# Kernel optimization log

Measured on AMD Instinct MI355X. Metric: run time of the kernel, lower is better.

The kernel has to match this reference:

```python
import jax, jax.numpy as jnp
import numpy as np
from jax import lax

SEQ_LEN = 1024
BATCH = 256
INPUT_SIZE = 64
STATE_SIZE = 960
STREAM_SIZE = INPUT_SIZE + STATE_SIZE  # 1024
OUTPUT_SIZE = 64
IDENTITY_PROPORTION = 0.97


def _xavier_uniform(key, shape):
    fan_in, fan_out = shape[1], shape[0]
    limit = np.sqrt(6.0 / (fan_in + fan_out)).astype(np.float32)
    return jax.random.uniform(key, shape, jnp.float32, -limit, limit)


def setup_inputs() -> dict:
    key = jax.random.key(0)
    k_x, k_w1, k_w2 = jax.random.split(key, 3)
    return {
        "input": jax.random.normal(k_x, (SEQ_LEN, BATCH, INPUT_SIZE), jnp.float32),
        "W1": _xavier_uniform(k_w1, (STREAM_SIZE, STREAM_SIZE)),
        "b1": jnp.zeros((STREAM_SIZE,), jnp.float32),
        "W2": _xavier_uniform(k_w2, (STREAM_SIZE, STREAM_SIZE)),
        "b2": jnp.zeros((STREAM_SIZE,), jnp.float32),
    }


def reference(input, W1, b1, W2, b2):
    p = jnp.asarray(IDENTITY_PROPORTION, input.dtype)

    def step(stream, x_t):
        # Shift: prepend new input, trim to stream width.
        # stream: (B, STREAM_SIZE), x_t: (B, INPUT_SIZE)
        s = jnp.concatenate([x_t, stream], axis=-1)[..., :STREAM_SIZE]
        # Res block: abs nonlinearity + residual mix.
        h = jnp.abs(s @ W1.T + b1)
        s = p * s + (1.0 - p) * (h @ W2.T + b2)
        return s, None

    init = jnp.zeros((input.shape[1], STREAM_SIZE), input.dtype)
    final_stream, _ = lax.scan(step, init, input)
    return final_stream[..., -OUTPUT_SIZE:]
```

## Files before the change

### kernel.cpp

```cpp
#include <hip/hip_runtime.h>
#include <hip/hip_bf16.h>
#include <stdint.h>


#define NSTEP  1024
#define BATCH  256
#define INSZ   64
#define SSZ    1024

#define GROUPS 8
#define CBLKS  32
#define RPG    32
#define CPB    32
#define FPAD   16
#define TSTR   36

typedef __bf16  bf16x8 __attribute__((ext_vector_type(8)));
typedef float   f32x4  __attribute__((ext_vector_type(4)));
typedef unsigned u32x2 __attribute__((ext_vector_type(2)));

#define SCHED_FENCE() __builtin_amdgcn_sched_barrier(0)
#define WAITN(n) do { asm volatile("s_waitcnt vmcnt(" #n ")" ::: "memory"); SCHED_FENCE(); } while (0)

__device__ __forceinline__ void issue8(const char* p,
    bf16x8& r0, bf16x8& r1, bf16x8& r2, bf16x8& r3,
    bf16x8& r4, bf16x8& r5, bf16x8& r6, bf16x8& r7)
{
    asm volatile(
        "global_load_dwordx4 %0, %8, off sc0 sc1\n\t"
        "global_load_dwordx4 %1, %8, off offset:64 sc0 sc1\n\t"
        "global_load_dwordx4 %2, %8, off offset:128 sc0 sc1\n\t"
        "global_load_dwordx4 %3, %8, off offset:192 sc0 sc1\n\t"
        "global_load_dwordx4 %4, %8, off offset:256 sc0 sc1\n\t"
        "global_load_dwordx4 %5, %8, off offset:320 sc0 sc1\n\t"
        "global_load_dwordx4 %6, %8, off offset:384 sc0 sc1\n\t"
        "global_load_dwordx4 %7, %8, off offset:448 sc0 sc1"
        : "=&v"(r0), "=&v"(r1), "=&v"(r2), "=&v"(r3),
          "=&v"(r4), "=&v"(r5), "=&v"(r6), "=&v"(r7)
        : "v"(p) : "memory");
}

__device__ __forceinline__ void issue4f(const float* p0, const float* p1,
                                        const float* p2, const float* p3,
                                        float& r0, float& r1, float& r2, float& r3)
{
    asm volatile(
        "global_load_dword %0, %4, off sc0 sc1\n\t"
        "global_load_dword %1, %5, off sc0 sc1\n\t"
        "global_load_dword %2, %6, off sc0 sc1\n\t"
        "global_load_dword %3, %7, off sc0 sc1"
        : "=&v"(r0), "=&v"(r1), "=&v"(r2), "=&v"(r3)
        : "v"(p0), "v"(p1), "v"(p2), "v"(p3)
        : "memory");
}

__device__ __forceinline__ void st_coh_u16(void* p, unsigned short v) {
    asm volatile("global_store_short %0, %1, off sc0 sc1" :: "v"(p), "v"(v) : "memory");
}
__device__ __forceinline__ void st_coh_f32(void* p, float v) {
    asm volatile("global_store_dword %0, %1, off sc0 sc1" :: "v"(p), "v"(v) : "memory");
}
__device__ __forceinline__ void st_coh_b64(void* p, u32x2 v) {
    asm volatile("global_store_dwordx2 %0, %1, off sc0 sc1" :: "v"(p), "v"(v) : "memory");
}
__device__ __forceinline__ void st_coh_b128(void* p, f32x4 v) {
    asm volatile("global_store_dwordx4 %0, %1, off sc0 sc1" :: "v"(p), "v"(v) : "memory");
}

__device__ __forceinline__ u32x2 pack_bf16x4(f32x4 f) {
    unsigned a = __builtin_bit_cast(unsigned short, (__bf16)f[0]);
    unsigned b = __builtin_bit_cast(unsigned short, (__bf16)f[1]);
    unsigned c = __builtin_bit_cast(unsigned short, (__bf16)f[2]);
    unsigned d = __builtin_bit_cast(unsigned short, (__bf16)f[3]);
    u32x2 r; r[0] = a | (b << 16); r[1] = c | (d << 16);
    return r;
}

__device__ __forceinline__ void group_barrier(unsigned* flags, int g, int c,
                                              unsigned e, int tid)
{
    asm volatile("s_waitcnt vmcnt(0)" ::: "memory");
    __syncthreads();
    if (tid == 0)
        __hip_atomic_store(&flags[(g * CBLKS + c) * FPAD], e, __ATOMIC_RELAXED,
                           __HIP_MEMORY_SCOPE_AGENT);
    if (tid < 64) {
        uint64_t t0 = __builtin_amdgcn_s_memrealtime();
        for (;;) {
            unsigned v = e;
            if (tid < CBLKS)
                v = __hip_atomic_load(&flags[(g * CBLKS + tid) * FPAD], __ATOMIC_RELAXED,
                                      __HIP_MEMORY_SCOPE_AGENT);
            if (!__any((int)(v - e) < 0)) break;
            if (__builtin_amdgcn_s_memrealtime() - t0 > 400000ull) break;
        }
    }
    __syncthreads();
}

#define MFMA8(BASE, A0, A1, A2, A3, A4, A5, A6, A7)                                        \
    do {                                                                                   \
        acc0 = __builtin_amdgcn_mfma_f32_16x16x32_bf16(A0,                                 \
            *reinterpret_cast<const bf16x8*>(Bw + ((((BASE) + 0) * 64 + kbyte) ^ bswz)),   \
            acc0, 0, 0, 0);                                                                \
        acc1 = __builtin_amdgcn_mfma_f32_16x16x32_bf16(A1,                                 \
            *reinterpret_cast<const bf16x8*>(Bw + ((((BASE) + 1) * 64 + kbyte) ^ bswz)),   \
            acc1, 0, 0, 0);                                                                \
        acc2 = __builtin_amdgcn_mfma_f32_16x16x32_bf16(A2,                                 \
            *reinterpret_cast<const bf16x8*>(Bw + ((((BASE) + 2) * 64 + kbyte) ^ bswz)),   \
            acc2, 0, 0, 0);                                                                \
        acc3 = __builtin_amdgcn_mfma_f32_16x16x32_bf16(A3,                                 \
            *reinterpret_cast<const bf16x8*>(Bw + ((((BASE) + 3) * 64 + kbyte) ^ bswz)),   \
            acc3, 0, 0, 0);                                                                \
        acc0 = __builtin_amdgcn_mfma_f32_16x16x32_bf16(A4,                                 \
            *reinterpret_cast<const bf16x8*>(Bw + ((((BASE) + 4) * 64 + kbyte) ^ bswz)),   \
            acc0, 0, 0, 0);                                                                \
        acc1 = __builtin_amdgcn_mfma_f32_16x16x32_bf16(A5,                                 \
            *reinterpret_cast<const bf16x8*>(Bw + ((((BASE) + 5) * 64 + kbyte) ^ bswz)),   \
            acc1, 0, 0, 0);                                                                \
        acc2 = __builtin_amdgcn_mfma_f32_16x16x32_bf16(A6,                                 \
            *reinterpret_cast<const bf16x8*>(Bw + ((((BASE) + 6) * 64 + kbyte) ^ bswz)),   \
            acc2, 0, 0, 0);                                                                \
        acc3 = __builtin_amdgcn_mfma_f32_16x16x32_bf16(A7,                                 \
            *reinterpret_cast<const bf16x8*>(Bw + ((((BASE) + 7) * 64 + kbyte) ^ bswz)),   \
            acc3, 0, 0, 0);                                                                \
    } while (0)

__device__ __forceinline__ f32x4 phase_mm(const char* Ab, const char* Bw,
                                          int kbyte, int bswz)
{
    f32x4 acc0 = {0.f, 0.f, 0.f, 0.f}, acc1 = acc0, acc2 = acc0, acc3 = acc0;
    bf16x8 a0, a1, a2, a3, a4, a5, a6, a7;
    bf16x8 b0, b1, b2, b3, b4, b5, b6, b7;
    bf16x8 e0, e1, e2, e3, e4, e5, e6, e7;
    bf16x8 d0, d1, d2, d3, d4, d5, d6, d7;

    issue8(Ab,        a0, a1, a2, a3, a4, a5, a6, a7);
    issue8(Ab +  512, b0, b1, b2, b3, b4, b5, b6, b7);
    issue8(Ab + 1024, e0, e1, e2, e3, e4, e5, e6, e7);
    issue8(Ab + 1536, d0, d1, d2, d3, d4, d5, d6, d7);
    WAITN(24); MFMA8(0,  a0, a1, a2, a3, a4, a5, a6, a7);
    WAITN(16); MFMA8(8,  b0, b1, b2, b3, b4, b5, b6, b7);
    WAITN(8);  MFMA8(16, e0, e1, e2, e3, e4, e5, e6, e7);
    WAITN(0);  MFMA8(24, d0, d1, d2, d3, d4, d5, d6, d7);

    return (acc0 + acc1) + (acc2 + acc3);
}

extern "C" __global__ void __launch_bounds__(256, 1)
resrnn_kernel(const float* __restrict__ x,  const float* __restrict__ W1,
              const float* __restrict__ b1, const float* __restrict__ W2,
              const float* __restrict__ b2,
              __bf16* sBuf, __bf16* hBuf, float* sf32, unsigned* flags,
              float* __restrict__ dout)
{
    extern __shared__ char smem[];
    char*  W1s = smem;
    char*  W2s = smem + 65536;
    float* T   = (float*)(smem + 131072);

    const int tid = threadIdx.x;
    const int bid = blockIdx.x;
    const int g   = bid & 7;
    const int c   = bid >> 3;
    const int rb  = g * RPG;
    const int cb  = c * CPB;

    {
        const int lcw = tid >> 3;
        const int seg = (tid & 7) * 128;
        const int sw  = (lcw & 7) << 4;
        const float* w1p = W1 + (size_t)(cb + lcw) * SSZ + seg;
        const float* w2p = W2 + (size_t)(cb + lcw) * SSZ + seg;
        char* d1 = W1s + lcw * 2048;
        char* d2 = W2s + lcw * 2048;
        #pragma unroll 4
        for (int kk = 0; kk < 16; ++kk) {
            const int kb = (seg + kk * 8) * 2;
            f32x4 f0 = reinterpret_cast<const f32x4*>(w1p)[kk * 2 + 0];
            f32x4 f1 = reinterpret_cast<const f32x4*>(w1p)[kk * 2 + 1];
            bf16x8 v;
            v[0] = (__bf16)f0[0]; v[1] = (__bf16)f0[1]; v[2] = (__bf16)f0[2]; v[3] = (__bf16)f0[3];
            v[4] = (__bf16)f1[0]; v[5] = (__bf16)f1[1]; v[6] = (__bf16)f1[2]; v[7] = (__bf16)f1[3];
            *reinterpret_cast<bf16x8*>(d1 + (kb ^ sw)) = v;
            f0 = reinterpret_cast<const f32x4*>(w2p)[kk * 2 + 0];
            f1 = reinterpret_cast<const f32x4*>(w2p)[kk * 2 + 1];
            v[0] = (__bf16)f0[0]; v[1] = (__bf16)f0[1]; v[2] = (__bf16)f0[2]; v[3] = (__bf16)f0[3];
            v[4] = (__bf16)f1[0]; v[5] = (__bf16)f1[1]; v[6] = (__bf16)f1[2]; v[7] = (__bf16)f1[3];
            *reinterpret_cast<bf16x8*>(d2 + (kb ^ sw)) = v;
        }
    }

    {
        const int e0  = tid * 4;
        const int row = rb + (e0 >> 5);
        const int col = cb + (e0 & 31);
        float* sp32 = sf32 + (size_t)row * SSZ + col;
        st_coh_f32(sp32 + 0, 0.f); st_coh_f32(sp32 + 1, 0.f);
        st_coh_f32(sp32 + 2, 0.f); st_coh_f32(sp32 + 3, 0.f);
        __bf16* sp = sBuf + (size_t)row * SSZ + col;
        if (c < 2) {
            const float* xp = x + (size_t)row * INSZ + col;
            #pragma unroll
            for (int i = 0; i < 4; ++i)
                st_coh_u16(sp + i, __builtin_bit_cast(unsigned short, (__bf16)xp[i]));
        } else {
            #pragma unroll
            for (int i = 0; i < 4; ++i)
                st_coh_u16(sp + i, __builtin_bit_cast(unsigned short, (__bf16)0.f));
        }
    }

    group_barrier(flags, g, c, 1u, tid);

    const int lane  = tid & 63;
    const int wv    = tid >> 6;
    const int mh    = wv >> 1;
    const int nh    = wv & 1;
    const int kgrp  = lane >> 4;
    const int kbyte = kgrp * 16;
    const int arow  = rb + mh * 16 + (lane & 15);
    const char* AbS = (const char*)sBuf + (size_t)arow * 2048 + kgrp * 16;
    const char* AbH = (const char*)hBuf + (size_t)arow * 2048 + kgrp * 16;
    const int lc    = nh * 16 + (lane & 15);
    const int bswz  = (lc & 7) << 4;
    const char* Bw1 = W1s + lc * 2048;
    const char* Bw2 = W2s + lc * 2048;
    const float bias1 = b1[cb + lc];
    const float bias2 = b2[cb + lc];
    const int lrow0 = mh * 16 + kgrp * 4;
    const int drow0 = rb + lrow0;
    const int dcol  = cb + lc;
    const float P = 0.97f, OMP = 1.0f - 0.97f;

    const int srow = tid >> 3;
    const int scol = (tid & 7) * 4;

    for (int t = 0; t < NSTEP; ++t) {
        {
            f32x4 h4 = phase_mm(AbS, Bw1, kbyte, bswz);
            #pragma unroll
            for (int j = 0; j < 4; ++j)
                T[(lrow0 + j) * TSTR + lc] = fabsf(h4[j] + bias1);
        }
        __syncthreads();
        {
            f32x4 hv = *reinterpret_cast<const f32x4*>(&T[srow * TSTR + scol]);
            st_coh_b64(hBuf + (size_t)(rb + srow) * SSZ + cb + scol, pack_bf16x4(hv));
        }

        const float* srd = sf32 + (size_t)(t & 1) * (BATCH * SSZ);
        float sp0, sp1, sp2, sp3;
        if (c < 2) {
            const float* xp = x + (size_t)t * (BATCH * INSZ);
            sp0 = xp[(size_t)(drow0 + 0) * INSZ + dcol];
            sp1 = xp[(size_t)(drow0 + 1) * INSZ + dcol];
            sp2 = xp[(size_t)(drow0 + 2) * INSZ + dcol];
            sp3 = xp[(size_t)(drow0 + 3) * INSZ + dcol];
        } else {
            issue4f(&srd[(size_t)(drow0 + 0) * SSZ + (dcol - 64)],
                    &srd[(size_t)(drow0 + 1) * SSZ + (dcol - 64)],
                    &srd[(size_t)(drow0 + 2) * SSZ + (dcol - 64)],
                    &srd[(size_t)(drow0 + 3) * SSZ + (dcol - 64)],
                    sp0, sp1, sp2, sp3);
        }

        group_barrier(flags, g, c, (unsigned)(2 + 2 * t), tid);

        {
            f32x4 u4 = phase_mm(AbH, Bw2, kbyte, bswz);
            const float spv[4] = {sp0, sp1, sp2, sp3};
            #pragma unroll
            for (int j = 0; j < 4; ++j)
                T[(lrow0 + j) * TSTR + lc] = P * spv[j] + OMP * (u4[j] + bias2);
        }
        __syncthreads();
        {
            float* swr = sf32 + (size_t)((t + 1) & 1) * (BATCH * SSZ);
            f32x4 sv  = *reinterpret_cast<const f32x4*>(&T[srow * TSTR + scol]);
            const int grow = rb + srow;
            st_coh_b128(&swr[(size_t)grow * SSZ + cb + scol], sv);
            if (c < 30) {
                st_coh_b64(sBuf + (size_t)grow * SSZ + (cb + 64) + scol, pack_bf16x4(sv));
            } else if (t == NSTEP - 1) {
                *reinterpret_cast<f32x4*>(&dout[grow * 64 + (cb - 960) + scol]) = sv;
            }
            if (c < 2 && t < NSTEP - 1) {
                f32x4 xv = *reinterpret_cast<const f32x4*>(
                    &x[(size_t)(t + 1) * (BATCH * INSZ) + (size_t)grow * INSZ + cb + scol]);
                st_coh_b64(sBuf + (size_t)grow * SSZ + cb + scol, pack_bf16x4(xv));
            }
        }
        if (t < NSTEP - 1)
            group_barrier(flags, g, c, (unsigned)(3 + 2 * t), tid);
    }
}

extern "C" void kernel_launch(void* const* d_in, const int* in_sizes, int n_in,
                              void* d_out, int out_size, void* d_ws, size_t ws_size,
                              hipStream_t stream)
{
    const float* x  = (const float*)d_in[0];
    const float* W1 = (const float*)d_in[1];
    const float* b1 = (const float*)d_in[2];
    const float* W2 = (const float*)d_in[3];
    const float* b2 = (const float*)d_in[4];
    float* dout = (float*)d_out;

    char* ws = (char*)d_ws;
    __bf16*   sBuf  = (__bf16*)(ws);
    __bf16*   hBuf  = (__bf16*)(ws + (512 << 10));
    float*    sf32  = (float*)(ws + (1 << 20));
    unsigned* flags = (unsigned*)(ws + (3 << 20));

    (void)in_sizes; (void)n_in; (void)out_size; (void)ws_size;

    (void)hipFuncSetAttribute(reinterpret_cast<const void*>(&resrnn_kernel),
                              hipFuncAttributeMaxDynamicSharedMemorySize, 135680);
    hipLaunchKernelGGL(resrnn_kernel, dim3(256), dim3(256), 135680, stream,
                       x, W1, b1, W2, b2, sBuf, hBuf, sf32, flags, dout);
}
```

Baseline: 10.90 ms.

## Split row group into two half-slots with separate flag sets to overlap barriers

Each block's 32 rows are split into two 16-row halves, each with its own flag array. While one half waits on its cross-block barrier, the other half's GEMM phase proceeds, hiding inter-block sync latency. The four waves now split K in two and reduce partial sums through shared memory instead of splitting M. This adds extra __syncthreads and LDS round-trips per phase, and doubles the number of flag publishes and waits.

```diff
diff --git a/kernel.cpp b/kernel.cpp
--- a/kernel.cpp
+++ b/kernel.cpp
@@ -11,13 +11,14 @@
 #define GROUPS 8
 #define CBLKS  32
 #define RPG    32
+#define RPH    16
 #define CPB    32
 #define FPAD   16
 #define TSTR   36
 
-typedef __bf16  bf16x8 __attribute__((ext_vector_type(8)));
-typedef float   f32x4  __attribute__((ext_vector_type(4)));
-typedef unsigned u32x2 __attribute__((ext_vector_type(2)));
+typedef __bf16   bf16x8 __attribute__((ext_vector_type(8)));
+typedef float    f32x4  __attribute__((ext_vector_type(4)));
+typedef unsigned u32x2  __attribute__((ext_vector_type(2)));
 
 #define SCHED_FENCE() __builtin_amdgcn_sched_barrier(0)
 #define WAITN(n) do { asm volatile("s_waitcnt vmcnt(" #n ")" ::: "memory"); SCHED_FENCE(); } while (0)
@@ -76,20 +77,23 @@
     return r;
 }
 
-__device__ __forceinline__ void group_barrier(unsigned* flags, int g, int c,
-                                              unsigned e, int tid)
+__device__ __forceinline__ void publish_flags(unsigned* fl, int c, unsigned e, int tid)
 {
     asm volatile("s_waitcnt vmcnt(0)" ::: "memory");
     __syncthreads();
     if (tid == 0)
-        __hip_atomic_store(&flags[(g * CBLKS + c) * FPAD], e, __ATOMIC_RELAXED,
+        __hip_atomic_store(&fl[c * FPAD], e, __ATOMIC_RELAXED,
                            __HIP_MEMORY_SCOPE_AGENT);
+}
+
+__device__ __forceinline__ void wait_flags(unsigned* fl, unsigned e, int tid)
+{
     if (tid < 64) {
         uint64_t t0 = __builtin_amdgcn_s_memrealtime();
         for (;;) {
             unsigned v = e;
             if (tid < CBLKS)
-                v = __hip_atomic_load(&flags[(g * CBLKS + tid) * FPAD], __ATOMIC_RELAXED,
+                v = __hip_atomic_load(&fl[tid * FPAD], __ATOMIC_RELAXED,
                                       __HIP_MEMORY_SCOPE_AGENT);
             if (!__any((int)(v - e) < 0)) break;
             if (__builtin_amdgcn_s_memrealtime() - t0 > 400000ull) break;
@@ -101,49 +105,33 @@
 #define MFMA8(BASE, A0, A1, A2, A3, A4, A5, A6, A7)                                        \
     do {                                                                                   \
         acc0 = __builtin_amdgcn_mfma_f32_16x16x32_bf16(A0,                                 \
-            *reinterpret_cast<const bf16x8*>(Bw + ((((BASE) + 0) * 64 + kbyte) ^ bswz)),   \
-            acc0, 0, 0, 0);                                                                \
+            *reinterpret_cast<const bf16x8*>(Bw + ((kboff + ((BASE) + 0) * 64 + kbyte) ^ bswz)), acc0, 0, 0, 0); \
         acc1 = __builtin_amdgcn_mfma_f32_16x16x32_bf16(A1,                                 \
-            *reinterpret_cast<const bf16x8*>(Bw + ((((BASE) + 1) * 64 + kbyte) ^ bswz)),   \
-            acc1, 0, 0, 0);                                                                \
+            *reinterpret_cast<const bf16x8*>(Bw + ((kboff + ((BASE) + 1) * 64 + kbyte) ^ bswz)), acc1, 0, 0, 0); \
         acc2 = __builtin_amdgcn_mfma_f32_16x16x32_bf16(A2,                                 \
-            *reinterpret_cast<const bf16x8*>(Bw + ((((BASE) + 2) * 64 + kbyte) ^ bswz)),   \
-            acc2, 0, 0, 0);                                                                \
+            *reinterpret_cast<const bf16x8*>(Bw + ((kboff + ((BASE) + 2) * 64 + kbyte) ^ bswz)), acc2, 0, 0, 0); \
         acc3 = __builtin_amdgcn_mfma_f32_16x16x32_bf16(A3,                                 \
-            *reinterpret_cast<const bf16x8*>(Bw + ((((BASE) + 3) * 64 + kbyte) ^ bswz)),   \
-            acc3, 0, 0, 0);                                                                \
+            *reinterpret_cast<const bf16x8*>(Bw + ((kboff + ((BASE) + 3) * 64 + kbyte) ^ bswz)), acc3, 0, 0, 0); \
         acc0 = __builtin_amdgcn_mfma_f32_16x16x32_bf16(A4,                                 \
-            *reinterpret_cast<const bf16x8*>(Bw + ((((BASE) + 4) * 64 + kbyte) ^ bswz)),   \
-            acc0, 0, 0, 0);                                                                \
+            *reinterpret_cast<const bf16x8*>(Bw + ((kboff + ((BASE) + 4) * 64 + kbyte) ^ bswz)), acc0, 0, 0, 0); \
         acc1 = __builtin_amdgcn_mfma_f32_16x16x32_bf16(A5,                                 \
-            *reinterpret_cast<const bf16x8*>(Bw + ((((BASE) + 5) * 64 + kbyte) ^ bswz)),   \
-            acc1, 0, 0, 0);                                                                \
+            *reinterpret_cast<const bf16x8*>(Bw + ((kboff + ((BASE) + 5) * 64 + kbyte) ^ bswz)), acc1, 0, 0, 0); \
         acc2 = __builtin_amdgcn_mfma_f32_16x16x32_bf16(A6,                                 \
-            *reinterpret_cast<const bf16x8*>(Bw + ((((BASE) + 6) * 64 + kbyte) ^ bswz)),   \
-            acc2, 0, 0, 0);                                                                \
+            *reinterpret_cast<const bf16x8*>(Bw + ((kboff + ((BASE) + 6) * 64 + kbyte) ^ bswz)), acc2, 0, 0, 0); \
         acc3 = __builtin_amdgcn_mfma_f32_16x16x32_bf16(A7,                                 \
-            *reinterpret_cast<const bf16x8*>(Bw + ((((BASE) + 7) * 64 + kbyte) ^ bswz)),   \
-            acc3, 0, 0, 0);                                                                \
+            *reinterpret_cast<const bf16x8*>(Bw + ((kboff + ((BASE) + 7) * 64 + kbyte) ^ bswz)), acc3, 0, 0, 0); \
     } while (0)
 
-__device__ __forceinline__ f32x4 phase_mm(const char* Ab, const char* Bw,
-                                          int kbyte, int bswz)
+__device__ __forceinline__ f32x4 phase_mm_half(const char* Ab, const char* Bw,
+                                               int kbyte, int bswz, int kboff)
 {
     f32x4 acc0 = {0.f, 0.f, 0.f, 0.f}, acc1 = acc0, acc2 = acc0, acc3 = acc0;
     bf16x8 a0, a1, a2, a3, a4, a5, a6, a7;
     bf16x8 b0, b1, b2, b3, b4, b5, b6, b7;
-    bf16x8 e0, e1, e2, e3, e4, e5, e6, e7;
-    bf16x8 d0, d1, d2, d3, d4, d5, d6, d7;
-
-    issue8(Ab,        a0, a1, a2, a3, a4, a5, a6, a7);
-    issue8(Ab +  512, b0, b1, b2, b3, b4, b5, b6, b7);
-    issue8(Ab + 1024, e0, e1, e2, e3, e4, e5, e6, e7);
-    issue8(Ab + 1536, d0, d1, d2, d3, d4, d5, d6, d7);
-    WAITN(24); MFMA8(0,  a0, a1, a2, a3, a4, a5, a6, a7);
-    WAITN(16); MFMA8(8,  b0, b1, b2, b3, b4, b5, b6, b7);
-    WAITN(8);  MFMA8(16, e0, e1, e2, e3, e4, e5, e6, e7);
-    WAITN(0);  MFMA8(24, d0, d1, d2, d3, d4, d5, d6, d7);
-
+    issue8(Ab,       a0, a1, a2, a3, a4, a5, a6, a7);
+    issue8(Ab + 512, b0, b1, b2, b3, b4, b5, b6, b7);
+    WAITN(8); MFMA8(0, a0, a1, a2, a3, a4, a5, a6, a7);
+    WAITN(0); MFMA8(8, b0, b1, b2, b3, b4, b5, b6, b7);
     return (acc0 + acc1) + (acc2 + acc3);
 }
 
@@ -211,74 +199,87 @@
         }
     }
 
-    group_barrier(flags, g, c, 1u, tid);
+    unsigned* flA = flags + (size_t)g * (CBLKS * FPAD);
+    unsigned* flB = flags + (size_t)(8 + g) * (CBLKS * FPAD);
+
+    asm volatile("s_waitcnt vmcnt(0)" ::: "memory");
+    __syncthreads();
+    if (tid == 0) {
+        __hip_atomic_store(&flA[c * FPAD], 1u, __ATOMIC_RELAXED, __HIP_MEMORY_SCOPE_AGENT);
+        __hip_atomic_store(&flB[c * FPAD], 1u, __ATOMIC_RELAXED, __HIP_MEMORY_SCOPE_AGENT);
+    }
+    wait_flags(flA, 1u, tid);
+    wait_flags(flB, 1u, tid);
 
     const int lane  = tid & 63;
     const int wv    = tid >> 6;
-    const int mh    = wv >> 1;
+    const int kh    = wv >> 1;
     const int nh    = wv & 1;
+    const int kboff = kh * 1024;
     const int kgrp  = lane >> 4;
     const int kbyte = kgrp * 16;
-    const int arow  = rb + mh * 16 + (lane & 15);
-    const char* AbS = (const char*)sBuf + (size_t)arow * 2048 + kgrp * 16;
-    const char* AbH = (const char*)hBuf + (size_t)arow * 2048 + kgrp * 16;
+    const int row16 = lane & 15;
     const int lc    = nh * 16 + (lane & 15);
     const int bswz  = (lc & 7) << 4;
     const char* Bw1 = W1s + lc * 2048;
     const char* Bw2 = W2s + lc * 2048;
     const float bias1 = b1[cb + lc];
     const float bias2 = b2[cb + lc];
-    const int lrow0 = mh * 16 + kgrp * 4;
-    const int drow0 = rb + lrow0;
+    const int lrow0 = kgrp * 4;
     const int dcol  = cb + lc;
     const float P = 0.97f, OMP = 1.0f - 0.97f;
 
     const int srow = tid >> 3;
     const int scol = (tid & 7) * 4;
 
-    for (int t = 0; t < NSTEP; ++t) {
-        {
-            f32x4 h4 = phase_mm(AbS, Bw1, kbyte, bswz);
-            #pragma unroll
-            for (int j = 0; j < 4; ++j)
-                T[(lrow0 + j) * TSTR + lc] = fabsf(h4[j] + bias1);
+    auto slot_p1 = [&](int half, int t, unsigned* fl) {
+        const char* Ab = (const char*)sBuf +
+            (size_t)(rb + half * RPH + row16) * 2048 + kboff + kbyte;
+        f32x4 part = phase_mm_half(Ab, Bw1, kbyte, bswz, kboff);
+        if (kh) {
+            #pragma unroll
+            for (int j = 0; j < 4; ++j) T[(lrow0 + j) * TSTR + lc] = part[j];
         }
         __syncthreads();
-        {
+        if (!kh) {
+            #pragma unroll
+            for (int j = 0; j < 4; ++j) {
+                const int idx = (lrow0 + j) * TSTR + lc;
+                T[idx] = fabsf(part[j] + T[idx] + bias1);
+            }
+        }
+        __syncthreads();
+        if (tid < 128) {
             f32x4 hv = *reinterpret_cast<const f32x4*>(&T[srow * TSTR + scol]);
-            st_coh_b64(hBuf + (size_t)(rb + srow) * SSZ + cb + scol, pack_bf16x4(hv));
-        }
-
-        const float* srd = sf32 + (size_t)(t & 1) * (BATCH * SSZ);
-        float sp0, sp1, sp2, sp3;
-        if (c < 2) {
-            const float* xp = x + (size_t)t * (BATCH * INSZ);
-            sp0 = xp[(size_t)(drow0 + 0) * INSZ + dcol];
-            sp1 = xp[(size_t)(drow0 + 1) * INSZ + dcol];
-            sp2 = xp[(size_t)(drow0 + 2) * INSZ + dcol];
-            sp3 = xp[(size_t)(drow0 + 3) * INSZ + dcol];
-        } else {
-            issue4f(&srd[(size_t)(drow0 + 0) * SSZ + (dcol - 64)],
-                    &srd[(size_t)(drow0 + 1) * SSZ + (dcol - 64)],
-                    &srd[(size_t)(drow0 + 2) * SSZ + (dcol - 64)],
-                    &srd[(size_t)(drow0 + 3) * SSZ + (dcol - 64)],
-                    sp0, sp1, sp2, sp3);
-        }
-
-        group_barrier(flags, g, c, (unsigned)(2 + 2 * t), tid);
-
-        {
-            f32x4 u4 = phase_mm(AbH, Bw2, kbyte, bswz);
+            const int grow = rb + half * RPH + srow;
+            st_coh_b64(hBuf + (size_t)grow * SSZ + cb + scol, pack_bf16x4(hv));
+        }
+        publish_flags(fl, c, (unsigned)(2 + 2 * t), tid);
+    };
+
+    auto slot_p2 = [&](int half, int t, unsigned* fl,
+                       float sp0, float sp1, float sp2, float sp3) {
+        const char* Ab = (const char*)hBuf +
+            (size_t)(rb + half * RPH + row16) * 2048 + kboff + kbyte;
+        f32x4 part = phase_mm_half(Ab, Bw2, kbyte, bswz, kboff);
+        if (kh) {
+            #pragma unroll
+            for (int j = 0; j < 4; ++j) T[(lrow0 + j) * TSTR + lc] = part[j];
+        }
+        __syncthreads();
+        if (!kh) {
             const float spv[4] = {sp0, sp1, sp2, sp3};
             #pragma unroll
-            for (int j = 0; j < 4; ++j)
-                T[(lrow0 + j) * TSTR + lc] = P * spv[j] + OMP * (u4[j] + bias2);
+            for (int j = 0; j < 4; ++j) {
+                const int idx = (lrow0 + j) * TSTR + lc;
+                T[idx] = P * spv[j] + OMP * (part[j] + T[idx] + bias2);
+            }
         }
         __syncthreads();
-        {
+        if (tid < 128) {
             float* swr = sf32 + (size_t)((t + 1) & 1) * (BATCH * SSZ);
-            f32x4 sv  = *reinterpret_cast<const f32x4*>(&T[srow * TSTR + scol]);
-            const int grow = rb + srow;
+            f32x4 sv = *reinterpret_cast<const f32x4*>(&T[srow * TSTR + scol]);
+            const int grow = rb + half * RPH + srow;
             st_coh_b128(&swr[(size_t)grow * SSZ + cb + scol], sv);
             if (c < 30) {
                 st_coh_b64(sBuf + (size_t)grow * SSZ + (cb + 64) + scol, pack_bf16x4(sv));
@@ -291,8 +292,47 @@
                 st_coh_b64(sBuf + (size_t)grow * SSZ + cb + scol, pack_bf16x4(xv));
             }
         }
+        publish_flags(fl, c, (unsigned)(3 + 2 * t), tid);
+    };
+
+    auto prefetch_sprev = [&](int half, int t,
+                              float& sp0, float& sp1, float& sp2, float& sp3) {
+        if (kh == 0) {
+            const int grow0 = rb + half * RPH + lrow0;
+            if (c < 2) {
+                const float* xp = x + (size_t)t * (BATCH * INSZ);
+                sp0 = xp[(size_t)(grow0 + 0) * INSZ + dcol];
+                sp1 = xp[(size_t)(grow0 + 1) * INSZ + dcol];
+                sp2 = xp[(size_t)(grow0 + 2) * INSZ + dcol];
+                sp3 = xp[(size_t)(grow0 + 3) * INSZ + dcol];
+            } else {
+                const float* srd = sf32 + (size_t)(t & 1) * (BATCH * SSZ);
+                issue4f(&srd[(size_t)(grow0 + 0) * SSZ + (dcol - 64)],
+                        &srd[(size_t)(grow0 + 1) * SSZ + (dcol - 64)],
+                        &srd[(size_t)(grow0 + 2) * SSZ + (dcol - 64)],
+                        &srd[(size_t)(grow0 + 3) * SSZ + (dcol - 64)],
+                        sp0, sp1, sp2, sp3);
+            }
+        }
+    };
+
+    for (int t = 0; t < NSTEP; ++t) {
+        slot_p1(0, t, flA);
+        wait_flags(flB, (unsigned)(1 + 2 * t), tid);
+        slot_p1(1, t, flB);
+
+        float a0, a1, a2, a3;
+        prefetch_sprev(0, t, a0, a1, a2, a3);
+        wait_flags(flA, (unsigned)(2 + 2 * t), tid);
+        slot_p2(0, t, flA, a0, a1, a2, a3);
+
+        float c0, c1, c2, c3;
+        prefetch_sprev(1, t, c0, c1, c2, c3);
+        wait_flags(flB, (unsigned)(2 + 2 * t), tid);
+        slot_p2(1, t, flB, c0, c1, c2, c3);
+
         if (t < NSTEP - 1)
-            group_barrier(flags, g, c, (unsigned)(3 + 2 * t), tid);
+            wait_flags(flA, (unsigned)(3 + 2 * t), tid);
     }
 }
 
@@ -316,7 +356,7 @@
     (void)in_sizes; (void)n_in; (void)out_size; (void)ws_size;
 
     (void)hipFuncSetAttribute(reinterpret_cast<const void*>(&resrnn_kernel),
-                              hipFuncAttributeMaxDynamicSharedMemorySize, 135680);
-    hipLaunchKernelGGL(resrnn_kernel, dim3(256), dim3(256), 135680, stream,
+                              hipFuncAttributeMaxDynamicSharedMemorySize, 133376);
+    hipLaunchKernelGGL(resrnn_kernel, dim3(256), dim3(256), 133376, stream,
                        x, W1, b1, W2, b2, sBuf, hBuf, sf32, flags, dout);
 }
```

Result: slower. 13.13 ms (+20.5%).
